# Optimization experiments

Measured on AMD Instinct MI355X. Metric: run time of the kernel, lower is better.

## Reference

```python
import jax, jax.numpy as jnp
import numpy as np

H = 16          # num_attention_heads
D_MODEL = 1024  # hidden_size
D_HEAD = D_MODEL // H


def setup_inputs() -> dict:
    key = jax.random.key(0)
    ks = jax.random.split(key, 8)
    B, S = 4, 2048
    s = 1.0 / np.sqrt(D_MODEL)
    return {
        "hidden_states": jax.random.normal(ks[0], (B, S, D_MODEL), jnp.float32),
        "attention_mask": jnp.zeros((B, 1, 1, S), jnp.float32),
        "Wq": jax.random.normal(ks[1], (D_MODEL, D_MODEL), jnp.float32) * s,
        "bq": jnp.zeros((D_MODEL,), jnp.float32),
        "Wk": jax.random.normal(ks[2], (D_MODEL, D_MODEL), jnp.float32) * s,
        "bk": jnp.zeros((D_MODEL,), jnp.float32),
        "Wv": jax.random.normal(ks[3], (D_MODEL, D_MODEL), jnp.float32) * s,
        "bv": jnp.zeros((D_MODEL,), jnp.float32),
    }


def reference(hidden_states, attention_mask, Wq, bq, Wk, bk, Wv, bv):
    B, S, _ = hidden_states.shape
    # QKV projections, split into heads: [B, H, S, d]
    def proj(W, b):
        x = hidden_states @ W + b
        return x.reshape(B, S, H, D_HEAD).transpose(0, 2, 1, 3)

    q = proj(Wq, bq)
    k = proj(Wk, bk)
    v = proj(Wv, bv)

    scores = jnp.einsum('bhqd,bhkd->bhqk', q, k) / np.sqrt(D_HEAD)
    scores = scores + attention_mask
    probs = jax.nn.softmax(scores, axis=-1)  # dropout prob = 0 (eval)
    ctx = jnp.einsum('bhqk,bhkd->bhqd', probs, v)
    return ctx.transpose(0, 2, 1, 3).reshape(B, S, D_MODEL)
```

## Files before the change

kernel.cpp:

```cpp
#include <hip/hip_runtime.h>
#include <hip/hip_bf16.h>


typedef float  f32x4  __attribute__((ext_vector_type(4)));
typedef float  f32x16 __attribute__((ext_vector_type(16)));
typedef short  short8 __attribute__((ext_vector_type(8)));
typedef __bf16 bf16x8 __attribute__((ext_vector_type(8)));
typedef unsigned int uint4v __attribute__((ext_vector_type(4)));

#define AS1 __attribute__((address_space(1)))
#define AS3 __attribute__((address_space(3)))

__device__ __forceinline__ void gload_lds16(const void* g, void* l) {
    __builtin_amdgcn_global_load_lds((const AS1 void*)g, (AS3 void*)l, 16, 0, 0);
}

__device__ __forceinline__ unsigned short f2bf(float f) {
    union { float f; unsigned int u; } v; v.f = f;
    unsigned int u = v.u;
    unsigned int r = (u + 0x7fffu + ((u >> 16) & 1u)) >> 16;
    return (unsigned short)r;
}

__device__ __forceinline__ unsigned packbf(float a, float b) {
    unsigned short lo = __builtin_bit_cast(unsigned short, (__bf16)a);
    unsigned short hh = __builtin_bit_cast(unsigned short, (__bf16)b);
    return (unsigned)lo | ((unsigned)hh << 16);
}

__device__ __forceinline__ f32x4 mfma16(short8 a, short8 b, f32x4 c) {
    return __builtin_amdgcn_mfma_f32_16x16x32_bf16(
        __builtin_bit_cast(bf16x8, a), __builtin_bit_cast(bf16x8, b), c, 0, 0, 0);
}

__device__ __forceinline__ f32x16 mfma32(short8 a, short8 b, f32x16 c) {
    return __builtin_amdgcn_mfma_f32_32x32x16_bf16(
        __builtin_bit_cast(bf16x8, a), __builtin_bit_cast(bf16x8, b), c, 0, 0, 0);
}

__device__ __forceinline__ f32x16 mfma32u(uint4v a, short8 b, f32x16 c) {
    return __builtin_amdgcn_mfma_f32_32x32x16_bf16(
        __builtin_bit_cast(bf16x8, a), __builtin_bit_cast(bf16x8, b), c, 0, 0, 0);
}


__global__ void conv_x(const float* __restrict__ X, unsigned short* __restrict__ Xb, int n4) {
    int i = blockIdx.x * blockDim.x + threadIdx.x;
    int stride = gridDim.x * blockDim.x;
    for (; i < n4; i += stride) {
        float4 v = ((const float4*)X)[i];
        ushort4 o;
        o.x = f2bf(v.x); o.y = f2bf(v.y); o.z = f2bf(v.z); o.w = f2bf(v.w);
        ((ushort4*)Xb)[i] = o;
    }
}

__global__ void conv_w_t(const float* __restrict__ Wq, const float* __restrict__ Wk,
                         const float* __restrict__ Wv,
                         unsigned short* __restrict__ Wqt, unsigned short* __restrict__ Wkt,
                         unsigned short* __restrict__ Wvt) {
    const float* W = (blockIdx.z == 0) ? Wq : (blockIdx.z == 1) ? Wk : Wv;
    unsigned short* Wt = (blockIdx.z == 0) ? Wqt : (blockIdx.z == 1) ? Wkt : Wvt;
    __shared__ unsigned short tile[64][65];
    int n0 = blockIdx.x * 64, k0 = blockIdx.y * 64;
    int t = threadIdx.x;
    int cr = t >> 6, cc = t & 63;
    for (int i = 0; i < 16; i++) {
        int row = i * 4 + cr;
        tile[row][cc] = f2bf(W[(size_t)(k0 + row) * 1024 + n0 + cc]);
    }
    __syncthreads();
    for (int i = 0; i < 16; i++) {
        int row = i * 4 + cr;
        Wt[(size_t)(n0 + row) * 1024 + k0 + cc] = tile[cc][row];
    }
}


__global__ __launch_bounds__(256)
void gemm_qk(const unsigned short* __restrict__ A,
             const unsigned short* __restrict__ Bt0, const unsigned short* __restrict__ Bt1,
             const float* __restrict__ bias0, const float* __restrict__ bias1,
             unsigned short* __restrict__ o0, unsigned short* __restrict__ o1) {
    __shared__ unsigned short Alds[2][4096];
    __shared__ unsigned short Blds[2][4096];
    const int K = 1024;
    const int z = blockIdx.z;
    const unsigned short* Bt = z ? Bt1 : Bt0;
    const float* bias = z ? bias1 : bias0;
    unsigned short* out = z ? o1 : o0;
    const float scale = z ? 1.0f : 0.125f;

    int t = threadIdx.x;
    int m0 = blockIdx.y * 128, n0 = blockIdx.x * 128;
    int wid = t >> 6, lane = t & 63, g = lane >> 4, r16 = lane & 15;
    int wr = wid >> 1, wc = wid & 1;

    f32x4 acc[4][4] = {};

    const unsigned short* Ab = A + (size_t)(m0 + (t >> 2)) * K + (t & 3) * 8;
    const unsigned short* Bb = Bt + (size_t)(n0 + (t >> 2)) * K + (t & 3) * 8;

#define STAGE_G(buf, k0)                                              \
    gload_lds16(Ab + (k0), &Alds[buf][wid * 512]);                    \
    gload_lds16(Ab + (k0) + (size_t)64 * K, &Alds[buf][2048 + wid * 512]); \
    gload_lds16(Bb + (k0), &Blds[buf][wid * 512]);                    \
    gload_lds16(Bb + (k0) + (size_t)64 * K, &Blds[buf][2048 + wid * 512]);

    STAGE_G(0, 0)
    asm volatile("s_waitcnt vmcnt(0)" ::: "memory");
    __syncthreads();

    int cur = 0;
    for (int k0 = 0; k0 < K; k0 += 32) {
        if (k0 + 32 < K) { STAGE_G(cur ^ 1, k0 + 32) }
        short8 af[4], bfr[4];
        #pragma unroll
        for (int m = 0; m < 4; m++)
            af[m] = *(const short8*)&Alds[cur][(wr * 64 + m * 16 + r16) * 32 + g * 8];
        #pragma unroll
        for (int n = 0; n < 4; n++)
            bfr[n] = *(const short8*)&Blds[cur][(wc * 64 + n * 16 + r16) * 32 + g * 8];
        #pragma unroll
        for (int m = 0; m < 4; m++)
            #pragma unroll
            for (int n = 0; n < 4; n++)
                acc[m][n] = mfma16(af[m], bfr[n], acc[m][n]);
        asm volatile("s_waitcnt vmcnt(0)" ::: "memory");
        __syncthreads();
        cur ^= 1;
    }

    for (int m = 0; m < 4; m++) {
        int gmBase = m0 + wr * 64 + m * 16 + g * 4;
        for (int n = 0; n < 4; n++) {
            int gn = n0 + wc * 64 + n * 16 + r16;
            float bcol = bias[gn];
            for (int r = 0; r < 4; r++) {
                int gm = gmBase + r;
                float v = (acc[m][n][r] + bcol) * scale;
                int b = gm >> 11, s = gm & 2047, h = gn >> 6, d = gn & 63;
                out[((size_t)(b * 16 + h) * 2048 + s) * 64 + d] = f2bf(v);
            }
        }
    }
}


__global__ __launch_bounds__(256)
void gemm_v(const unsigned short* __restrict__ A, const unsigned short* __restrict__ Bt,
            const float* __restrict__ bias, unsigned short* __restrict__ out) {
    __shared__ unsigned short Alds[2][4096];
    __shared__ unsigned short Blds[2][4096];
    const int K = 1024, N = 8192;

    int t = threadIdx.x;
    int m0 = blockIdx.y * 128, n0 = blockIdx.x * 128;
    int wid = t >> 6, lane = t & 63, g = lane >> 4, r16 = lane & 15;
    int wr = wid >> 1, wc = wid & 1;

    f32x4 acc[4][4] = {};

    const unsigned short* Ab = A + (size_t)(m0 + (t >> 2)) * K + (t & 3) * 8;
    const unsigned short* Bb = Bt + (size_t)(n0 + (t >> 2)) * K + (t & 3) * 8;

    STAGE_G(0, 0)
    asm volatile("s_waitcnt vmcnt(0)" ::: "memory");
    __syncthreads();

    int cur = 0;
    for (int k0 = 0; k0 < K; k0 += 32) {
        if (k0 + 32 < K) { STAGE_G(cur ^ 1, k0 + 32) }
        short8 af[4], bfr[4];
        #pragma unroll
        for (int m = 0; m < 4; m++)
            af[m] = *(const short8*)&Alds[cur][(wr * 64 + m * 16 + r16) * 32 + g * 8];
        #pragma unroll
        for (int n = 0; n < 4; n++)
            bfr[n] = *(const short8*)&Blds[cur][(wc * 64 + n * 16 + r16) * 32 + g * 8];
        #pragma unroll
        for (int m = 0; m < 4; m++)
            #pragma unroll
            for (int n = 0; n < 4; n++)
                acc[m][n] = mfma16(af[m], bfr[n], acc[m][n]);
        asm volatile("s_waitcnt vmcnt(0)" ::: "memory");
        __syncthreads();
        cur ^= 1;
    }

    for (int m = 0; m < 4; m++) {
        int gmBase = m0 + wr * 64 + m * 16 + g * 4;
        for (int n = 0; n < 4; n++) {
            int gn = n0 + wc * 64 + n * 16 + r16;
            for (int r = 0; r < 4; r++) {
                int gm = gmBase + r;
                out[(size_t)gm * N + gn] = f2bf(acc[m][n][r] + bias[gm]);
            }
        }
    }
}


__global__ __launch_bounds__(256, 2)
void attn(const unsigned short* __restrict__ Qb, const unsigned short* __restrict__ Kb,
          const unsigned short* __restrict__ Vtb, const float* __restrict__ mask,
          float* __restrict__ out) {
    __shared__ unsigned short Kl[2][4096];
    __shared__ unsigned short Vl[2][4096];
    __shared__ float sums[4][64];

    const int t = threadIdx.x, wid = t >> 6, lane = t & 63;
    const int hi = lane >> 5, c = lane & 31;
    const int bh = blockIdx.x, b = bh >> 4, h = bh & 15;
    const int q0w = blockIdx.y * 256 + wid * 64;

    short8 qf[2][4];
    #pragma unroll
    for (int qh = 0; qh < 2; qh++)
        #pragma unroll
        for (int ds = 0; ds < 4; ds++)
            qf[qh][ds] = *(const short8*)&Qb[((size_t)bh * 2048 + q0w + qh * 32 + c) * 64
                                             + ds * 16 + hi * 8];

    float lsum[2] = {0.f, 0.f};
    f32x16 ctx[2][2] = {};

    const int srow = t >> 3, schk = (t & 7) ^ (srow & 7);
    const unsigned short* Kst = Kb + (size_t)bh * 2048 * 64 + srow * 64 + schk * 8;
    const unsigned short* Vst = Vtb + (size_t)(h * 64 + srow) * 8192 + (size_t)b * 2048 + schk * 8;
    const float* mrow = mask + (size_t)b * 2048;

    gload_lds16(Kst,                       &Kl[0][wid * 512]);
    gload_lds16(Kst + (size_t)32 * 64,     &Kl[0][2048 + wid * 512]);
    gload_lds16(Vst,                       &Vl[0][wid * 512]);
    gload_lds16(Vst + (size_t)32 * 8192,   &Vl[0][2048 + wid * 512]);
    asm volatile("s_waitcnt vmcnt(0)" ::: "memory");
    __syncthreads();

    int cur = 0;
    for (int t0 = 0; t0 < 2048; t0 += 64) {
        if (t0 + 64 < 2048) {
            const unsigned short* nK = Kst + (size_t)(t0 + 64) * 64;
            const unsigned short* nV = Vst + (t0 + 64);
            gload_lds16(nK,                     &Kl[cur ^ 1][wid * 512]);
            gload_lds16(nK + (size_t)32 * 64,   &Kl[cur ^ 1][2048 + wid * 512]);
            gload_lds16(nV,                     &Vl[cur ^ 1][wid * 512]);
            gload_lds16(nV + (size_t)32 * 8192, &Vl[cur ^ 1][2048 + wid * 512]);
        }
        const unsigned short* K_ = Kl[cur];
        const unsigned short* V_ = Vl[cur];

        uint4v pa[2][4];
        #pragma unroll
        for (int kb = 0; kb < 2; kb++) {
            short8 kf[4];
            #pragma unroll
            for (int ds = 0; ds < 4; ds++) {
                const int row = kb * 32 + c;
                kf[ds] = *(const short8*)&K_[row * 64 + (((ds * 2 + hi) ^ (row & 7)) * 8)];
            }
            float4 m4[4];
            #pragma unroll
            for (int q = 0; q < 4; q++)
                m4[q] = *(const float4*)&mrow[t0 + kb * 32 + q * 8 + hi * 4];
            #pragma unroll
            for (int qh = 0; qh < 2; qh++) {
                f32x16 st;
                #pragma unroll
                for (int q = 0; q < 4; q++) {
                    st[q * 4 + 0] = m4[q].x; st[q * 4 + 1] = m4[q].y;
                    st[q * 4 + 2] = m4[q].z; st[q * 4 + 3] = m4[q].w;
                }
                #pragma unroll
                for (int ds = 0; ds < 4; ds++)
                    st = mfma32(kf[ds], qf[qh][ds], st);
                float p[16];
                #pragma unroll
                for (int r = 0; r < 16; r++) {
                    p[r] = __expf(st[r]);
                    lsum[qh] += p[r];
                }
                unsigned cc[8], sx[8];
                #pragma unroll
                for (int i = 0; i < 8; i++) cc[i] = packbf(p[2 * i], p[2 * i + 1]);
                #pragma unroll
                for (int i = 0; i < 8; i++) sx[i] = __shfl_xor(cc[i], 32);
                pa[qh][kb * 2] = (uint4v){
                    hi ? sx[2] : cc[0], hi ? sx[3] : cc[1],
                    hi ? cc[2] : sx[0], hi ? cc[3] : sx[1]};
                pa[qh][kb * 2 + 1] = (uint4v){
                    hi ? sx[6] : cc[4], hi ? sx[7] : cc[5],
                    hi ? cc[6] : sx[4], hi ? cc[7] : sx[5]};
            }
        }
        #pragma unroll
        for (int db = 0; db < 2; db++) {
            #pragma unroll
            for (int ts = 0; ts < 4; ts++) {
                const int row = db * 32 + c;
                short8 vf = *(const short8*)&V_[row * 64 + (((ts * 2 + hi) ^ (row & 7)) * 8)];
                ctx[0][db] = mfma32u(pa[0][ts], vf, ctx[0][db]);
                ctx[1][db] = mfma32u(pa[1][ts], vf, ctx[1][db]);
            }
        }
        asm volatile("s_waitcnt vmcnt(0)" ::: "memory");
        __syncthreads();
        cur ^= 1;
    }

    #pragma unroll
    for (int qh = 0; qh < 2; qh++) {
        float tot = lsum[qh] + __shfl_xor(lsum[qh], 32);
        if (hi == 0) sums[wid][qh * 32 + c] = tot;
    }
    __syncthreads();
    #pragma unroll
    for (int qh = 0; qh < 2; qh++) {
        #pragma unroll
        for (int rg = 0; rg < 4; rg++) {
            float4 sv = *(const float4*)&sums[wid][qh * 32 + rg * 8 + hi * 4];
            float svf[4] = {sv.x, sv.y, sv.z, sv.w};
            #pragma unroll
            for (int r = 0; r < 4; r++) {
                const float inv = 1.f / svf[r];
                const int reg = rg * 4 + r;
                const int row = q0w + qh * 32 + rg * 8 + hi * 4 + r;
                out[((size_t)b * 2048 + row) * 1024 + h * 64 + c]      = ctx[qh][0][reg] * inv;
                out[((size_t)b * 2048 + row) * 1024 + h * 64 + 32 + c] = ctx[qh][1][reg] * inv;
            }
        }
    }
}


extern "C" void kernel_launch(void* const* d_in, const int* in_sizes, int n_in,
                              void* d_out, int out_size, void* d_ws, size_t ws_size,
                              hipStream_t stream) {
    const float* X    = (const float*)d_in[0];
    const float* mask = (const float*)d_in[1];
    const float* Wq   = (const float*)d_in[2];
    const float* bq   = (const float*)d_in[3];
    const float* Wk   = (const float*)d_in[4];
    const float* bk   = (const float*)d_in[5];
    const float* Wv   = (const float*)d_in[6];
    const float* bv   = (const float*)d_in[7];
    float* out = (float*)d_out;

    unsigned short* ws  = (unsigned short*)d_ws;
    unsigned short* Xb  = ws;
    unsigned short* Wqt = Xb + 8388608;
    unsigned short* Wkt = Wqt + 1048576;
    unsigned short* Wvt = Wkt + 1048576;
    unsigned short* Qb  = Wvt + 1048576;
    unsigned short* Kb  = Qb + 8388608;
    unsigned short* Vtb = Kb + 8388608;

    conv_x<<<2048, 256, 0, stream>>>(X, Xb, 2097152);
    conv_w_t<<<dim3(16, 16, 3), 256, 0, stream>>>(Wq, Wk, Wv, Wqt, Wkt, Wvt);

    gemm_qk<<<dim3(8, 64, 2), 256, 0, stream>>>(Xb, Wqt, Wkt, bq, bk, Qb, Kb);
    gemm_v<<<dim3(64, 8), 256, 0, stream>>>(Wvt, Xb, bv, Vtb);

    attn<<<dim3(64, 8), 256, 0, stream>>>(Qb, Kb, Vtb, mask, out);
}
```

Measured before the change: 278.8 us.

## Double KV tile to 128 keys, interleave PV per 32-key block, halve shuffles

The attention loop now stages 128 keys per iteration instead of 64, which halves the number of barrier and wait points, and re-lays the V tile as 64 rows by 128 columns with a wider swizzle. The PV MFMAs now run right after each 32-key score block instead of after all of them, which shortens the live range of the probability fragments. The cross-half lane exchange sends one shuffle per pair of words instead of two, and s_setprio is raised around the MFMA bursts. LDS use doubles to 64KB per block, which may limit how many blocks fit per CU.

```diff
diff --git a/kernel.cpp b/kernel.cpp
--- a/kernel.cpp
+++ b/kernel.cpp
@@ -205,8 +205,8 @@
 void attn(const unsigned short* __restrict__ Qb, const unsigned short* __restrict__ Kb,
           const unsigned short* __restrict__ Vtb, const float* __restrict__ mask,
           float* __restrict__ out) {
-    __shared__ unsigned short Kl[2][4096];
-    __shared__ unsigned short Vl[2][4096];
+    __shared__ unsigned short Kl[2][8192];
+    __shared__ unsigned short Vl[2][8192];
     __shared__ float sums[4][64];
 
     const int t = threadIdx.x, wid = t >> 6, lane = t & 63;
@@ -225,44 +225,47 @@
     float lsum[2] = {0.f, 0.f};
     f32x16 ctx[2][2] = {};
 
-    const int srow = t >> 3, schk = (t & 7) ^ (srow & 7);
+    const int srow = t >> 3;
+    const int schk = (t & 7) ^ (srow & 7);
     const unsigned short* Kst = Kb + (size_t)bh * 2048 * 64 + srow * 64 + schk * 8;
-    const unsigned short* Vst = Vtb + (size_t)(h * 64 + srow) * 8192 + (size_t)b * 2048 + schk * 8;
+    const int vd = t >> 4;
+    const int vchk = (t & 15) ^ (vd & 7);
+    const unsigned short* Vst = Vtb + (size_t)(h * 64 + vd) * 8192 + (size_t)b * 2048 + vchk * 8;
     const float* mrow = mask + (size_t)b * 2048;
 
-    gload_lds16(Kst,                       &Kl[0][wid * 512]);
-    gload_lds16(Kst + (size_t)32 * 64,     &Kl[0][2048 + wid * 512]);
-    gload_lds16(Vst,                       &Vl[0][wid * 512]);
-    gload_lds16(Vst + (size_t)32 * 8192,   &Vl[0][2048 + wid * 512]);
+#define STAGE_KV(buf, T0)                                                         \
+    gload_lds16(Kst + (size_t)(T0) * 64,         &Kl[buf][wid * 512]);            \
+    gload_lds16(Kst + (size_t)((T0) + 32) * 64,  &Kl[buf][2048 + wid * 512]);     \
+    gload_lds16(Kst + (size_t)((T0) + 64) * 64,  &Kl[buf][4096 + wid * 512]);     \
+    gload_lds16(Kst + (size_t)((T0) + 96) * 64,  &Kl[buf][6144 + wid * 512]);     \
+    gload_lds16(Vst + (T0),                      &Vl[buf][wid * 512]);            \
+    gload_lds16(Vst + (T0) + (size_t)16 * 8192,  &Vl[buf][2048 + wid * 512]);     \
+    gload_lds16(Vst + (T0) + (size_t)32 * 8192,  &Vl[buf][4096 + wid * 512]);     \
+    gload_lds16(Vst + (T0) + (size_t)48 * 8192,  &Vl[buf][6144 + wid * 512]);
+
+    STAGE_KV(0, 0)
     asm volatile("s_waitcnt vmcnt(0)" ::: "memory");
     __syncthreads();
 
     int cur = 0;
-    for (int t0 = 0; t0 < 2048; t0 += 64) {
-        if (t0 + 64 < 2048) {
-            const unsigned short* nK = Kst + (size_t)(t0 + 64) * 64;
-            const unsigned short* nV = Vst + (t0 + 64);
-            gload_lds16(nK,                     &Kl[cur ^ 1][wid * 512]);
-            gload_lds16(nK + (size_t)32 * 64,   &Kl[cur ^ 1][2048 + wid * 512]);
-            gload_lds16(nV,                     &Vl[cur ^ 1][wid * 512]);
-            gload_lds16(nV + (size_t)32 * 8192, &Vl[cur ^ 1][2048 + wid * 512]);
-        }
+    for (int t0 = 0; t0 < 2048; t0 += 128) {
+        if (t0 + 128 < 2048) { STAGE_KV(cur ^ 1, t0 + 128) }
         const unsigned short* K_ = Kl[cur];
         const unsigned short* V_ = Vl[cur];
 
-        uint4v pa[2][4];
-        #pragma unroll
-        for (int kb = 0; kb < 2; kb++) {
+        #pragma unroll
+        for (int kb = 0; kb < 4; kb++) {
+            const int krow = kb * 32 + c;
             short8 kf[4];
             #pragma unroll
-            for (int ds = 0; ds < 4; ds++) {
-                const int row = kb * 32 + c;
-                kf[ds] = *(const short8*)&K_[row * 64 + (((ds * 2 + hi) ^ (row & 7)) * 8)];
-            }
+            for (int ds = 0; ds < 4; ds++)
+                kf[ds] = *(const short8*)&K_[krow * 64 + (((ds * 2 + hi) ^ (krow & 7)) * 8)];
             float4 m4[4];
             #pragma unroll
             for (int q = 0; q < 4; q++)
                 m4[q] = *(const float4*)&mrow[t0 + kb * 32 + q * 8 + hi * 4];
+
+            uint4v pa[2][2];
             #pragma unroll
             for (int qh = 0; qh < 2; qh++) {
                 f32x16 st;
@@ -271,38 +274,55 @@
                     st[q * 4 + 0] = m4[q].x; st[q * 4 + 1] = m4[q].y;
                     st[q * 4 + 2] = m4[q].z; st[q * 4 + 3] = m4[q].w;
                 }
+                __builtin_amdgcn_s_setprio(1);
                 #pragma unroll
                 for (int ds = 0; ds < 4; ds++)
                     st = mfma32(kf[ds], qf[qh][ds], st);
+                __builtin_amdgcn_s_setprio(0);
                 float p[16];
                 #pragma unroll
                 for (int r = 0; r < 16; r++) {
                     p[r] = __expf(st[r]);
                     lsum[qh] += p[r];
                 }
-                unsigned cc[8], sx[8];
+                unsigned cc[8];
                 #pragma unroll
                 for (int i = 0; i < 8; i++) cc[i] = packbf(p[2 * i], p[2 * i + 1]);
-                #pragma unroll
-                for (int i = 0; i < 8; i++) sx[i] = __shfl_xor(cc[i], 32);
-                pa[qh][kb * 2] = (uint4v){
-                    hi ? sx[2] : cc[0], hi ? sx[3] : cc[1],
-                    hi ? cc[2] : sx[0], hi ? cc[3] : sx[1]};
-                pa[qh][kb * 2 + 1] = (uint4v){
-                    hi ? sx[6] : cc[4], hi ? sx[7] : cc[5],
-                    hi ? cc[6] : sx[4], hi ? cc[7] : sx[5]};
-            }
+                unsigned w[8];
+                #pragma unroll
+                for (int i = 0; i < 2; i++) {
+                    {
+                        unsigned u = hi ? cc[i] : cc[i + 2];
+                        unsigned s = __shfl_xor(u, 32);
+                        w[i]     = hi ? s : cc[i];
+                        w[i + 2] = hi ? cc[i + 2] : s;
+                    }
+                    {
+                        unsigned u = hi ? cc[i + 4] : cc[i + 6];
+                        unsigned s = __shfl_xor(u, 32);
+                        w[i + 4] = hi ? s : cc[i + 4];
+                        w[i + 6] = hi ? cc[i + 6] : s;
+                    }
+                }
+                pa[qh][0] = (uint4v){w[0], w[1], w[2], w[3]};
+                pa[qh][1] = (uint4v){w[4], w[5], w[6], w[7]};
+            }
+
+            __builtin_amdgcn_s_setprio(1);
+            #pragma unroll
+            for (int db = 0; db < 2; db++) {
+                const int vrow = db * 32 + c;
+                #pragma unroll
+                for (int tl = 0; tl < 2; tl++) {
+                    const int chunk = (kb * 2 + tl) * 2 + hi;
+                    short8 vf = *(const short8*)&V_[vrow * 128 + ((chunk ^ (vrow & 7)) * 8)];
+                    ctx[0][db] = mfma32u(pa[0][tl], vf, ctx[0][db]);
+                    ctx[1][db] = mfma32u(pa[1][tl], vf, ctx[1][db]);
+                }
+            }
+            __builtin_amdgcn_s_setprio(0);
         }
-        #pragma unroll
-        for (int db = 0; db < 2; db++) {
-            #pragma unroll
-            for (int ts = 0; ts < 4; ts++) {
-                const int row = db * 32 + c;
-                short8 vf = *(const short8*)&V_[row * 64 + (((ts * 2 + hi) ^ (row & 7)) * 8)];
-                ctx[0][db] = mfma32u(pa[0][ts], vf, ctx[0][db]);
-                ctx[1][db] = mfma32u(pa[1][ts], vf, ctx[1][db]);
-            }
-        }
+
         asm volatile("s_waitcnt vmcnt(0)" ::: "memory");
         __syncthreads();
         cur ^= 1;
```

New measurement: 279.9 us. No clear change (+0.4%).
